# Performance work log

Measured on AMD Instinct MI355X. Metric: run time of the kernel, lower is better.

## Reference

```python
import jax, jax.numpy as jnp
import numpy as np
import math

B, L, D = 4, 2048, 512
H = 8
HD = D // H
K1 = 64  # local_window_size
K2 = 64  # global_window_size


def semi_local_mask(seq_len):
    # Faithful to create_semi_local_mask: anti-diagonal band + global prefix, ANDed with causal tril.
    i = jnp.arange(seq_len)[:, None]
    j = jnp.arange(seq_len)[None, :]
    band = (i + j >= seq_len - K1) & (i + j <= seq_len)
    glob = (j <= K2) & (j <= seq_len - i)
    causal = j <= i
    return (band | glob) & causal  # [L, L] bool


def setup_inputs() -> dict:
    key = jax.random.key(0)
    ks = jax.random.split(key, 8)
    def xavier(k, shape):
        fan_in, fan_out = shape[1], shape[0]
        lim = math.sqrt(6.0 / (fan_in + fan_out))
        return jax.random.uniform(k, shape, jnp.float32, -lim, lim)
    x = jax.random.normal(ks[0], (B, L, D), jnp.float32)
    w_qkv = xavier(ks[1], (3 * D, D)); b_qkv = jnp.zeros((3 * D,), jnp.float32)
    w_u = xavier(ks[2], (D, D));       b_u = jnp.zeros((D,), jnp.float32)
    w_out = xavier(ks[3], (D, D));     b_out = jnp.zeros((D,), jnp.float32)
    return {"x": x, "w_qkv": w_qkv, "b_qkv": b_qkv, "w_u": w_u, "b_u": b_u,
            "w_out": w_out, "b_out": b_out}


def reference(x, w_qkv, b_qkv, w_u, b_u, w_out, b_out):
    Bsz, Lq, Dm = x.shape
    qkv = (x @ w_qkv.T + b_qkv).reshape(Bsz, Lq, 3, H, HD)
    q, k, v = jnp.moveaxis(qkv, 2, 0)            # each [B, L, H, HD]
    q = jnp.transpose(q, (0, 2, 1, 3))           # [B, H, L, HD]
    k = jnp.transpose(k, (0, 2, 1, 3))
    v = jnp.transpose(v, (0, 2, 1, 3))
    u = x @ w_u.T + b_u                          # [B, L, D] (gate values)
    scale = 1.0 / math.sqrt(HD)
    scores = jnp.einsum('bhqd,bhkd->bhqk', q * scale, k)
    mask = semi_local_mask(Lq)                   # [L, L]
    scores = jnp.where(mask[None, None], scores, -jnp.inf)
    attn = jax.nn.softmax(scores, axis=-1)
    out = jnp.einsum('bhqk,bhkd->bhqd', attn, v)
    out = jnp.transpose(out, (0, 2, 1, 3)).reshape(Bsz, Lq, Dm)
    out = jax.nn.silu(out) * u
    return out @ w_out.T + b_out
```

## Files before the change

kernel.cpp:

```cpp
#include <hip/hip_runtime.h>
#include <hip/hip_bf16.h>

typedef __bf16 bf16x8 __attribute__((ext_vector_type(8)));
typedef float f32x4 __attribute__((ext_vector_type(4)));

#define B_ 4
#define L_ 2048
#define D_ 512
#define H_ 8
#define QS 2048
#define SP 72

#define SB0 __builtin_amdgcn_sched_barrier(0)
#define WAIT_VM(n) asm volatile("s_waitcnt vmcnt(" #n ")" ::: "memory")
#define WAIT_LGKM0 asm volatile("s_waitcnt lgkmcnt(0)" ::: "memory")

__device__ __forceinline__ void gl16(const __bf16* g, __bf16* l) {
  __builtin_amdgcn_global_load_lds(
      (const __attribute__((address_space(1))) void*)g,
      (__attribute__((address_space(3))) void*)l, 16, 0, 0);
}

__global__ __launch_bounds__(256) void cvt_pack(
    const float* __restrict__ x, const float* __restrict__ wq,
    const float* __restrict__ wu, const float* __restrict__ wo,
    const float* __restrict__ bq, const float* __restrict__ bu,
    __bf16* __restrict__ xb, __bf16* __restrict__ wcat,
    __bf16* __restrict__ wob, float* __restrict__ bcat)
{
  const int idx8 = blockIdx.x * 256 + threadIdx.x;
  const float* src; __bf16* dst; size_t so, dof;
  if (idx8 < 524288)      { src = x;  dst = xb;   so = (size_t)idx8 * 8;            dof = so; }
  else if (idx8 < 622592) { src = wq; dst = wcat; so = (size_t)(idx8 - 524288) * 8; dof = so; }
  else if (idx8 < 655360) { src = wu; dst = wcat; so = (size_t)(idx8 - 622592) * 8; dof = so + 786432; }
  else                    { src = wo; dst = wob;  so = (size_t)(idx8 - 655360) * 8; dof = so; }
  const float4 lo = *(const float4*)(src + so);
  const float4 hi = *(const float4*)(src + so + 4);
  bf16x8 r;
  r[0] = (__bf16)lo.x; r[1] = (__bf16)lo.y; r[2] = (__bf16)lo.z; r[3] = (__bf16)lo.w;
  r[4] = (__bf16)hi.x; r[5] = (__bf16)hi.y; r[6] = (__bf16)hi.z; r[7] = (__bf16)hi.w;
  *(bf16x8*)(dst + dof) = r;
  if (blockIdx.x == 0) {
#pragma unroll
    for (int e = 0; e < 8; ++e) {
      const int col = threadIdx.x * 8 + e;
      bcat[col] = (col < 1536) ? bq[col] : bu[col - 1536];
    }
  }
}

__global__ __launch_bounds__(256, 2) void gemm128(
    const __bf16* __restrict__ A, const __bf16* __restrict__ W,
    const float* __restrict__ bias, __bf16* __restrict__ C,
    int M, int N, int K)
{
  extern __shared__ char sm[];
  const int t = threadIdx.x;
  const int lane = t & 63;
  const int wave = t >> 6;
  const int wm = (wave >> 1) * 64;
  const int wn = (wave & 1) * 64;
  const int bm0 = blockIdx.x * 128;
  const int bn0 = blockIdx.y * 128;
  const int r = lane & 15, q = lane >> 4;
  const int nt = K >> 6;

  auto stage = [&](int kt, int p) {
#pragma unroll
    for (int j = 0; j < 4; ++j) {
      const int c = t + j * 256;
      const int row = c >> 3;
      const int cs = (c & 7) ^ (row & 7);
      gl16(A + (size_t)(bm0 + row) * K + kt * 64 + cs * 8,
           (__bf16*)(sm + p * 16384) + c * 8);
    }
#pragma unroll
    for (int j = 0; j < 4; ++j) {
      const int c = t + j * 256;
      const int row = c >> 3;
      const int cs = (c & 7) ^ (row & 7);
      gl16(W + (size_t)(bn0 + row) * K + kt * 64 + cs * 8,
           (__bf16*)(sm + 32768 + p * 16384) + c * 8);
    }
  };
  auto rdA = [&](int p, int mi, int ks) -> bf16x8 {
    const int row = wm + mi * 16 + r;
    const int byte = row * 128 + ((ks * 64 + q * 16) ^ ((row & 7) << 4));
    return *(const bf16x8*)(sm + p * 16384 + byte);
  };
  auto rdB = [&](int p, int ni, int ks) -> bf16x8 {
    const int row = wn + ni * 16 + r;
    const int byte = row * 128 + ((ks * 64 + q * 16) ^ ((row & 7) << 4));
    return *(const bf16x8*)(sm + 32768 + p * 16384 + byte);
  };

  f32x4 acc[4][4] = {};
  stage(0, 0);
  stage(1, 1);

  for (int kt = 0; kt < nt - 1; ++kt) {
    const int p = kt & 1;
    WAIT_VM(8);
    SB0; __builtin_amdgcn_s_barrier(); SB0;

    bf16x8 a[4][2], b01[2][2], b23[2][2];
#pragma unroll
    for (int mi = 0; mi < 4; ++mi) { a[mi][0] = rdA(p, mi, 0); a[mi][1] = rdA(p, mi, 1); }
#pragma unroll
    for (int ni = 0; ni < 2; ++ni) { b01[ni][0] = rdB(p, ni, 0); b01[ni][1] = rdB(p, ni, 1); }
    __builtin_amdgcn_s_setprio(1);
#pragma unroll
    for (int mi = 0; mi < 4; ++mi)
#pragma unroll
      for (int ni = 0; ni < 2; ++ni) {
        acc[mi][ni] = __builtin_amdgcn_mfma_f32_16x16x32_bf16(a[mi][0], b01[ni][0], acc[mi][ni], 0, 0, 0);
        acc[mi][ni] = __builtin_amdgcn_mfma_f32_16x16x32_bf16(a[mi][1], b01[ni][1], acc[mi][ni], 0, 0, 0);
      }
    __builtin_amdgcn_s_setprio(0);
#pragma unroll
    for (int ni = 0; ni < 2; ++ni) { b23[ni][0] = rdB(p, ni + 2, 0); b23[ni][1] = rdB(p, ni + 2, 1); }
    WAIT_LGKM0;
    SB0; __builtin_amdgcn_s_barrier(); SB0;
    if (kt + 2 < nt) stage(kt + 2, p);
    __builtin_amdgcn_s_setprio(1);
#pragma unroll
    for (int mi = 0; mi < 4; ++mi)
#pragma unroll
      for (int ni = 0; ni < 2; ++ni) {
        acc[mi][ni + 2] = __builtin_amdgcn_mfma_f32_16x16x32_bf16(a[mi][0], b23[ni][0], acc[mi][ni + 2], 0, 0, 0);
        acc[mi][ni + 2] = __builtin_amdgcn_mfma_f32_16x16x32_bf16(a[mi][1], b23[ni][1], acc[mi][ni + 2], 0, 0, 0);
      }
    __builtin_amdgcn_s_setprio(0);
  }

  {
    const int p = (nt - 1) & 1;
    const int cc = lane & 15, cq = lane >> 4;
    WAIT_VM(0);
    SB0; __builtin_amdgcn_s_barrier(); SB0;

    float bv[4];
#pragma unroll
    for (int ni = 0; ni < 4; ++ni) bv[ni] = bias[bn0 + wn + ni * 16 + cc];

    auto st = [&](int mi, int ni) {
      const int gcol = bn0 + wn + ni * 16 + cc;
#pragma unroll
      for (int rr = 0; rr < 4; ++rr) {
        const int grow = bm0 + wm + mi * 16 + cq * 4 + rr;
        C[(size_t)grow * N + gcol] = (__bf16)(acc[mi][ni][rr] + bv[ni]);
      }
    };

    bf16x8 a[4][2], b01[2][2], b23[2][2];
#pragma unroll
    for (int mi = 0; mi < 4; ++mi) { a[mi][0] = rdA(p, mi, 0); a[mi][1] = rdA(p, mi, 1); }
#pragma unroll
    for (int ni = 0; ni < 2; ++ni) { b01[ni][0] = rdB(p, ni, 0); b01[ni][1] = rdB(p, ni, 1); }
    __builtin_amdgcn_s_setprio(1);
#pragma unroll
    for (int mi = 0; mi < 4; ++mi)
#pragma unroll
      for (int ni = 0; ni < 2; ++ni) {
        acc[mi][ni] = __builtin_amdgcn_mfma_f32_16x16x32_bf16(a[mi][0], b01[ni][0], acc[mi][ni], 0, 0, 0);
        acc[mi][ni] = __builtin_amdgcn_mfma_f32_16x16x32_bf16(a[mi][1], b01[ni][1], acc[mi][ni], 0, 0, 0);
      }
    __builtin_amdgcn_s_setprio(0);
#pragma unroll
    for (int mi = 0; mi < 4; ++mi)
#pragma unroll
      for (int ni = 0; ni < 2; ++ni) st(mi, ni);

#pragma unroll
    for (int ni = 0; ni < 2; ++ni) { b23[ni][0] = rdB(p, ni + 2, 0); b23[ni][1] = rdB(p, ni + 2, 1); }
    __builtin_amdgcn_s_setprio(1);
#pragma unroll
    for (int mi = 0; mi < 4; ++mi)
#pragma unroll
      for (int ni = 0; ni < 2; ++ni) {
        acc[mi][ni + 2] = __builtin_amdgcn_mfma_f32_16x16x32_bf16(a[mi][0], b23[ni][0], acc[mi][ni + 2], 0, 0, 0);
        acc[mi][ni + 2] = __builtin_amdgcn_mfma_f32_16x16x32_bf16(a[mi][1], b23[ni][1], acc[mi][ni + 2], 0, 0, 0);
      }
    __builtin_amdgcn_s_setprio(0);
#pragma unroll
    for (int mi = 0; mi < 4; ++mi)
#pragma unroll
      for (int ni = 2; ni < 4; ++ni) st(mi, ni);
  }
}

__global__ __launch_bounds__(256, 2) void gemm_out(
    const __bf16* __restrict__ A, const __bf16* __restrict__ W,
    const float* __restrict__ bias, float* __restrict__ C)
{
  __shared__ char sm[49152];
  const int t = threadIdx.x;
  const int lane = t & 63;
  const int wave = t >> 6;
  const int wm = (wave >> 1) * 32;
  const int wn = (wave & 1) * 64;
  const int bm0 = blockIdx.x * 64;
  const int bn0 = blockIdx.y * 128;
  const int r = lane & 15, q = lane >> 4;
  const int K = 512, N = 512;

  auto stage = [&](int kt, int p) {
#pragma unroll
    for (int j = 0; j < 2; ++j) {
      const int c = t + j * 256;
      const int row = c >> 3;
      const int cs = (c & 7) ^ (row & 7);
      gl16(A + (size_t)(bm0 + row) * K + kt * 64 + cs * 8,
           (__bf16*)(sm + p * 8192) + c * 8);
    }
#pragma unroll
    for (int j = 0; j < 4; ++j) {
      const int c = t + j * 256;
      const int row = c >> 3;
      const int cs = (c & 7) ^ (row & 7);
      gl16(W + (size_t)(bn0 + row) * K + kt * 64 + cs * 8,
           (__bf16*)(sm + 16384 + p * 16384) + c * 8);
    }
  };
  auto rdA = [&](int p, int mi, int ks) -> bf16x8 {
    const int row = wm + mi * 16 + r;
    const int byte = row * 128 + ((ks * 64 + q * 16) ^ ((row & 7) << 4));
    return *(const bf16x8*)(sm + p * 8192 + byte);
  };
  auto rdB = [&](int p, int ni, int ks) -> bf16x8 {
    const int row = wn + ni * 16 + r;
    const int byte = row * 128 + ((ks * 64 + q * 16) ^ ((row & 7) << 4));
    return *(const bf16x8*)(sm + 16384 + p * 16384 + byte);
  };

  f32x4 acc[2][4] = {};
  stage(0, 0);
  stage(1, 1);

  for (int kt = 0; kt < 7; ++kt) {
    const int p = kt & 1;
    WAIT_VM(6);
    SB0; __builtin_amdgcn_s_barrier(); SB0;

    bf16x8 a[2][2], b01[2][2], b23[2][2];
#pragma unroll
    for (int mi = 0; mi < 2; ++mi) { a[mi][0] = rdA(p, mi, 0); a[mi][1] = rdA(p, mi, 1); }
#pragma unroll
    for (int ni = 0; ni < 2; ++ni) { b01[ni][0] = rdB(p, ni, 0); b01[ni][1] = rdB(p, ni, 1); }
    __builtin_amdgcn_s_setprio(1);
#pragma unroll
    for (int mi = 0; mi < 2; ++mi)
#pragma unroll
      for (int ni = 0; ni < 2; ++ni) {
        acc[mi][ni] = __builtin_amdgcn_mfma_f32_16x16x32_bf16(a[mi][0], b01[ni][0], acc[mi][ni], 0, 0, 0);
        acc[mi][ni] = __builtin_amdgcn_mfma_f32_16x16x32_bf16(a[mi][1], b01[ni][1], acc[mi][ni], 0, 0, 0);
      }
    __builtin_amdgcn_s_setprio(0);
#pragma unroll
    for (int ni = 0; ni < 2; ++ni) { b23[ni][0] = rdB(p, ni + 2, 0); b23[ni][1] = rdB(p, ni + 2, 1); }
    WAIT_LGKM0;
    SB0; __builtin_amdgcn_s_barrier(); SB0;
    if (kt + 2 < 8) stage(kt + 2, p);
    __builtin_amdgcn_s_setprio(1);
#pragma unroll
    for (int mi = 0; mi < 2; ++mi)
#pragma unroll
      for (int ni = 0; ni < 2; ++ni) {
        acc[mi][ni + 2] = __builtin_amdgcn_mfma_f32_16x16x32_bf16(a[mi][0], b23[ni][0], acc[mi][ni + 2], 0, 0, 0);
        acc[mi][ni + 2] = __builtin_amdgcn_mfma_f32_16x16x32_bf16(a[mi][1], b23[ni][1], acc[mi][ni + 2], 0, 0, 0);
      }
    __builtin_amdgcn_s_setprio(0);
  }

  {
    const int p = 1;
    const int cc = lane & 15, cq = lane >> 4;
    WAIT_VM(0);
    SB0; __builtin_amdgcn_s_barrier(); SB0;

    float bv[4];
#pragma unroll
    for (int ni = 0; ni < 4; ++ni) bv[ni] = bias[bn0 + wn + ni * 16 + cc];

    auto st = [&](int mi, int ni) {
      const int gcol = bn0 + wn + ni * 16 + cc;
#pragma unroll
      for (int rr = 0; rr < 4; ++rr) {
        const int grow = bm0 + wm + mi * 16 + cq * 4 + rr;
        C[(size_t)grow * N + gcol] = acc[mi][ni][rr] + bv[ni];
      }
    };

    bf16x8 a[2][2], b01[2][2], b23[2][2];
#pragma unroll
    for (int mi = 0; mi < 2; ++mi) { a[mi][0] = rdA(p, mi, 0); a[mi][1] = rdA(p, mi, 1); }
#pragma unroll
    for (int ni = 0; ni < 2; ++ni) { b01[ni][0] = rdB(p, ni, 0); b01[ni][1] = rdB(p, ni, 1); }
    __builtin_amdgcn_s_setprio(1);
#pragma unroll
    for (int mi = 0; mi < 2; ++mi)
#pragma unroll
      for (int ni = 0; ni < 2; ++ni) {
        acc[mi][ni] = __builtin_amdgcn_mfma_f32_16x16x32_bf16(a[mi][0], b01[ni][0], acc[mi][ni], 0, 0, 0);
        acc[mi][ni] = __builtin_amdgcn_mfma_f32_16x16x32_bf16(a[mi][1], b01[ni][1], acc[mi][ni], 0, 0, 0);
      }
    __builtin_amdgcn_s_setprio(0);
#pragma unroll
    for (int mi = 0; mi < 2; ++mi)
#pragma unroll
      for (int ni = 0; ni < 2; ++ni) st(mi, ni);

#pragma unroll
    for (int ni = 0; ni < 2; ++ni) { b23[ni][0] = rdB(p, ni + 2, 0); b23[ni][1] = rdB(p, ni + 2, 1); }
    __builtin_amdgcn_s_setprio(1);
#pragma unroll
    for (int mi = 0; mi < 2; ++mi)
#pragma unroll
      for (int ni = 0; ni < 2; ++ni) {
        acc[mi][ni + 2] = __builtin_amdgcn_mfma_f32_16x16x32_bf16(a[mi][0], b23[ni][0], acc[mi][ni + 2], 0, 0, 0);
        acc[mi][ni + 2] = __builtin_amdgcn_mfma_f32_16x16x32_bf16(a[mi][1], b23[ni][1], acc[mi][ni + 2], 0, 0, 0);
      }
    __builtin_amdgcn_s_setprio(0);
#pragma unroll
    for (int mi = 0; mi < 2; ++mi)
#pragma unroll
      for (int ni = 2; ni < 4; ++ni) st(mi, ni);
  }
}

__global__ __launch_bounds__(512) void attn_tile(
    const __bf16* __restrict__ qu,
    __bf16* __restrict__ g)
{
  const int qt = blockIdx.x, h = blockIdx.y, b = blockIdx.z;
  const int t = threadIdx.x;
  const int lane = t & 63;
  const int w = t >> 6;
  const int q0 = qt * 128, qmax = q0 + 127;
  const size_t bL = (size_t)b * L_;

  __shared__ __bf16 lK[4096];
  __shared__ __bf16 lV[64 * SP];
  __shared__ __bf16 Pb[128 * SP];

  const int cq = lane >> 4, cc = lane & 15;
  const int krow_st = t >> 3, kgb8 = t & 7;

  bf16x8 aq0, aq1;
  {
    const __bf16* qsrc = qu + (bL + q0 + w * 16 + cc) * QS + h * 64 + cq * 8;
    bf16x8 t0 = *(const bf16x8*)qsrc;
    bf16x8 t1 = *(const bf16x8*)(qsrc + 32);
#pragma unroll
    for (int e = 0; e < 8; ++e) {
      aq0[e] = (__bf16)((float)t0[e] * 0.125f);
      aq1[e] = (__bf16)((float)t1[e] * 0.125f);
    }
  }

  float mreg[4], lreg[4];
#pragma unroll
  for (int rr = 0; rr < 4; ++rr) { mreg[rr] = -1e30f; lreg[rr] = 0.f; }
  f32x4 acc_o[4] = {};

  int clist[8]; int ncl = 0;
  clist[ncl++] = 0;
  if (qmax >= 64) clist[ncl++] = 64;
  {
    int lo = 1984 - qmax; if (lo < 0) lo = 0; lo &= ~63;
    const int hik = min(qmax, 2048 - q0);
    for (int c = lo; c <= hik; c += 64)
      if (c >= 128) clist[ncl++] = c;
  }

  bf16x8 k0r, var;
  {
    const __bf16* src = qu + (bL + clist[0] + krow_st) * QS + 512 + h * 64;
    k0r = *(const bf16x8*)(src + kgb8 * 8);
    const __bf16* vsrc = qu + (bL + clist[0] + lane) * QS + 1024 + h * 64 + w * 8;
    var = *(const bf16x8*)vsrc;
  }

  for (int ci = 0; ci < ncl; ++ci) {
    const int c0 = clist[ci];
    const bool thin = (c0 == 64) && (qmax <= 1856);
    const bool fast0 = (c0 == 0) && (q0 >= 64) && (qmax + 63 <= 2048);

    WAIT_VM(0);
    SB0; __builtin_amdgcn_s_barrier(); SB0;
    {
      char* lkb = (char*)lK;
      const int sw = (krow_st & 7) << 4;
      *(bf16x8*)(lkb + ((krow_st * 128 + kgb8 * 16) ^ sw)) = k0r;
#pragma unroll
      for (int e = 0; e < 8; ++e)
        lV[(w * 8 + e) * SP + lane] = var[e];
    }
    if (ci + 1 < ncl) {
      const int cn = clist[ci + 1];
      const __bf16* src = qu + (bL + cn + krow_st) * QS + 512 + h * 64;
      k0r = *(const bf16x8*)(src + kgb8 * 8);
      const __bf16* vsrc = qu + (bL + cn + lane) * QS + 1024 + h * 64 + w * 8;
      var = *(const bf16x8*)vsrc;
    }
    WAIT_LGKM0;
    SB0; __builtin_amdgcn_s_barrier(); SB0;

    f32x4 s[4];
    {
      const char* lkb = (const char*)lK;
      auto qk = [&](int nt) {
        const int krow = nt * 16 + cc;
        const int sw = (krow & 7) << 4;
        bf16x8 bk0 = *(const bf16x8*)(lkb + ((krow * 128 + cq * 16) ^ sw));
        bf16x8 bk1 = *(const bf16x8*)(lkb + ((krow * 128 + 64 + cq * 16) ^ sw));
        f32x4 a = {};
        a = __builtin_amdgcn_mfma_f32_16x16x32_bf16(aq0, bk0, a, 0, 0, 0);
        a = __builtin_amdgcn_mfma_f32_16x16x32_bf16(aq1, bk1, a, 0, 0, 0);
        s[nt] = a;
      };
      qk(0);
      if (!thin) { qk(1); qk(2); qk(3); }
    }

    if (!fast0) {
      const int ntm = thin ? 1 : 4;
      if (c0 >= 128) {
        for (int nt = 0; nt < 4; ++nt) {
          if (nt >= ntm) break;
#pragma unroll
          for (int rr = 0; rr < 4; ++rr) {
            const int i = q0 + w * 16 + cq * 4 + rr;
            const int j = c0 + nt * 16 + cc;
            const int ij = i + j;
            const bool valid = (j <= i) && (ij >= 1984) && (ij <= 2048);
            s[nt][rr] = valid ? s[nt][rr] : -1e30f;
          }
        }
      } else {
        for (int nt = 0; nt < 4; ++nt) {
          if (nt >= ntm) break;
#pragma unroll
          for (int rr = 0; rr < 4; ++rr) {
            const int i = q0 + w * 16 + cq * 4 + rr;
            const int j = c0 + nt * 16 + cc;
            const int ij = i + j;
            const bool valid = (j <= i) &&
                ((ij >= 1984 && ij <= 2048) || (j <= 64 && ij <= 2048));
            s[nt][rr] = valid ? s[nt][rr] : -1e30f;
          }
        }
      }
    }

    f32x4 pm;
#pragma unroll
    for (int rr = 0; rr < 4; ++rr) pm[rr] = s[0][rr];
    if (!thin) {
#pragma unroll
      for (int rr = 0; rr < 4; ++rr)
        pm[rr] = fmaxf(fmaxf(pm[rr], s[1][rr]), fmaxf(s[2][rr], s[3][rr]));
    }
#pragma unroll
    for (int m = 1; m < 16; m <<= 1) {
#pragma unroll
      for (int rr = 0; rr < 4; ++rr)
        pm[rr] = fmaxf(pm[rr], __shfl_xor(pm[rr], m, 64));
    }
    float corr[4];
#pragma unroll
    for (int rr = 0; rr < 4; ++rr) {
      const float nm = fmaxf(mreg[rr], pm[rr]);
      corr[rr] = __expf(mreg[rr] - nm);
      mreg[rr] = nm;
    }

    f32x4 ps = {};
    if (thin) {
#pragma unroll
      for (int rr = 0; rr < 4; ++rr) {
        const float p = __expf(s[0][rr] - mreg[rr]);
        ps[rr] += p;
        const int prow = (w * 16 + cq * 4 + rr) * SP;
        Pb[prow + cc] = (__bf16)p;
        Pb[prow + 16 + cc] = (__bf16)0.f;
      }
    } else {
#pragma unroll
      for (int nt = 0; nt < 4; ++nt) {
#pragma unroll
        for (int rr = 0; rr < 4; ++rr) {
          const float p = __expf(s[nt][rr] - mreg[rr]);
          ps[rr] += p;
          Pb[(w * 16 + cq * 4 + rr) * SP + nt * 16 + cc] = (__bf16)p;
        }
      }
    }
#pragma unroll
    for (int m = 1; m < 16; m <<= 1) {
#pragma unroll
      for (int rr = 0; rr < 4; ++rr)
        ps[rr] += __shfl_xor(ps[rr], m, 64);
    }
#pragma unroll
    for (int rr = 0; rr < 4; ++rr) lreg[rr] = lreg[rr] * corr[rr] + ps[rr];

    {
      bf16x8 pa0 = *(const bf16x8*)(Pb + (w * 16 + cc) * SP + cq * 8);
      if (thin) {
#pragma unroll
        for (int dt = 0; dt < 4; ++dt) {
#pragma unroll
          for (int rr = 0; rr < 4; ++rr) acc_o[dt][rr] *= corr[rr];
          bf16x8 vb0 = *(const bf16x8*)(lV + (dt * 16 + cc) * SP + cq * 8);
          acc_o[dt] = __builtin_amdgcn_mfma_f32_16x16x32_bf16(pa0, vb0, acc_o[dt], 0, 0, 0);
        }
      } else {
        bf16x8 pa1 = *(const bf16x8*)(Pb + (w * 16 + cc) * SP + 32 + cq * 8);
#pragma unroll
        for (int dt = 0; dt < 4; ++dt) {
#pragma unroll
          for (int rr = 0; rr < 4; ++rr) acc_o[dt][rr] *= corr[rr];
          bf16x8 vb0 = *(const bf16x8*)(lV + (dt * 16 + cc) * SP + cq * 8);
          bf16x8 vb1 = *(const bf16x8*)(lV + (dt * 16 + cc) * SP + 32 + cq * 8);
          acc_o[dt] = __builtin_amdgcn_mfma_f32_16x16x32_bf16(pa0, vb0, acc_o[dt], 0, 0, 0);
          acc_o[dt] = __builtin_amdgcn_mfma_f32_16x16x32_bf16(pa1, vb1, acc_o[dt], 0, 0, 0);
        }
      }
    }
  }

#pragma unroll
  for (int dt = 0; dt < 4; ++dt) {
#pragma unroll
    for (int rr = 0; rr < 4; ++rr) {
      const int row16 = cq * 4 + rr;
      const size_t qrow = bL + q0 + w * 16 + row16;
      const int d = dt * 16 + cc;
      const float o = acc_o[dt][rr] / fmaxf(lreg[rr], 1e-30f);
      const float uv = (float)qu[qrow * QS + 1536 + h * 64 + d];
      g[qrow * D_ + h * 64 + d] = (__bf16)(o / (1.f + __expf(-o)) * uv);
    }
  }
}

extern "C" void kernel_launch(void* const* d_in, const int* in_sizes, int n_in,
                              void* d_out, int out_size, void* d_ws, size_t ws_size,
                              hipStream_t stream) {
  const float* x     = (const float*)d_in[0];
  const float* w_qkv = (const float*)d_in[1];
  const float* b_qkv = (const float*)d_in[2];
  const float* w_u   = (const float*)d_in[3];
  const float* b_u   = (const float*)d_in[4];
  const float* w_out = (const float*)d_in[5];
  const float* b_out = (const float*)d_in[6];
  float* out = (float*)d_out;

  char* ws = (char*)d_ws;
  __bf16* xb   = (__bf16*)ws;
  __bf16* wcat = (__bf16*)(ws + 8388608);
  __bf16* wob  = (__bf16*)(ws + 10485760);
  float*  bcat = (float*) (ws + 11010048);
  __bf16* qu   = (__bf16*)(ws + 11018240);
  __bf16* gb   = (__bf16*)(ws + 44572672);

  static bool attr_done = []() {
    hipFuncSetAttribute((const void*)gemm128,
                        hipFuncAttributeMaxDynamicSharedMemorySize, 65536);
    return true;
  }();
  (void)attr_done;

  cvt_pack<<<dim3(2688), dim3(256), 0, stream>>>(
      x, w_qkv, w_u, w_out, b_qkv, b_u, xb, wcat, wob, bcat);
  gemm128<<<dim3(64, 16), dim3(256), 65536, stream>>>(
      xb, wcat, bcat, qu, 8192, 2048, 512);
  attn_tile<<<dim3(L_ / 128, H_, B_), dim3(512), 0, stream>>>(qu, gb);
  gemm_out<<<dim3(128, 4), dim3(256), 0, stream>>>(
      gb, wob, b_out, out);
}
```

Before: 136.7 us.

## Fuse fp32-to-bf16 conversion of x into the QKV/U projection GEMM

Instead of a separate pass that converts x to bf16 in workspace, the projection GEMM now loads fp32 x rows into registers, converts them, and writes bf16 into LDS, with a register double-buffer and a fully unrolled K loop. The conversion kernel only handles the weights now. This removes an 8 MB bf16 write and reread of x. The cost is that each x tile is read as fp32 by all 16 column blocks (twice the bytes per load), plus extra register pressure and VALU work inside the GEMM.

```diff
diff --git a/kernel.cpp b/kernel.cpp
--- a/kernel.cpp
+++ b/kernel.cpp
@@ -22,18 +22,16 @@
 }
 
 __global__ __launch_bounds__(256) void cvt_pack(
-    const float* __restrict__ x, const float* __restrict__ wq,
-    const float* __restrict__ wu, const float* __restrict__ wo,
-    const float* __restrict__ bq, const float* __restrict__ bu,
-    __bf16* __restrict__ xb, __bf16* __restrict__ wcat,
+    const float* __restrict__ wq, const float* __restrict__ wu,
+    const float* __restrict__ wo, const float* __restrict__ bq,
+    const float* __restrict__ bu, __bf16* __restrict__ wcat,
     __bf16* __restrict__ wob, float* __restrict__ bcat)
 {
   const int idx8 = blockIdx.x * 256 + threadIdx.x;
   const float* src; __bf16* dst; size_t so, dof;
-  if (idx8 < 524288)      { src = x;  dst = xb;   so = (size_t)idx8 * 8;            dof = so; }
-  else if (idx8 < 622592) { src = wq; dst = wcat; so = (size_t)(idx8 - 524288) * 8; dof = so; }
-  else if (idx8 < 655360) { src = wu; dst = wcat; so = (size_t)(idx8 - 622592) * 8; dof = so + 786432; }
-  else                    { src = wo; dst = wob;  so = (size_t)(idx8 - 655360) * 8; dof = so; }
+  if (idx8 < 98304)       { src = wq; dst = wcat; so = (size_t)idx8 * 8;            dof = so; }
+  else if (idx8 < 131072) { src = wu; dst = wcat; so = (size_t)(idx8 - 98304) * 8;  dof = so + 786432; }
+  else                    { src = wo; dst = wob;  so = (size_t)(idx8 - 131072) * 8; dof = so; }
   const float4 lo = *(const float4*)(src + so);
   const float4 hi = *(const float4*)(src + so + 4);
   bf16x8 r;
@@ -49,10 +47,9 @@
   }
 }
 
-__global__ __launch_bounds__(256, 2) void gemm128(
-    const __bf16* __restrict__ A, const __bf16* __restrict__ W,
-    const float* __restrict__ bias, __bf16* __restrict__ C,
-    int M, int N, int K)
+__global__ __launch_bounds__(256, 2) void gemm_qkvu(
+    const float* __restrict__ X, const __bf16* __restrict__ W,
+    const float* __restrict__ bias, __bf16* __restrict__ C)
 {
   extern __shared__ char sm[];
   const int t = threadIdx.x;
@@ -63,24 +60,39 @@
   const int bm0 = blockIdx.x * 128;
   const int bn0 = blockIdx.y * 128;
   const int r = lane & 15, q = lane >> 4;
-  const int nt = K >> 6;
-
-  auto stage = [&](int kt, int p) {
+  const int N = 2048;
+
+  auto stageA = [&](int kt, f32x4 (&ar)[8]) {
 #pragma unroll
     for (int j = 0; j < 4; ++j) {
       const int c = t + j * 256;
       const int row = c >> 3;
       const int cs = (c & 7) ^ (row & 7);
-      gl16(A + (size_t)(bm0 + row) * K + kt * 64 + cs * 8,
-           (__bf16*)(sm + p * 16384) + c * 8);
-    }
+      const float* src = X + (size_t)(bm0 + row) * 512 + kt * 64 + cs * 8;
+      ar[2 * j]     = *(const f32x4*)src;
+      ar[2 * j + 1] = *(const f32x4*)(src + 4);
+    }
+  };
+  auto stageB = [&](int kt, int p) {
 #pragma unroll
     for (int j = 0; j < 4; ++j) {
       const int c = t + j * 256;
       const int row = c >> 3;
       const int cs = (c & 7) ^ (row & 7);
-      gl16(W + (size_t)(bn0 + row) * K + kt * 64 + cs * 8,
+      gl16(W + (size_t)(bn0 + row) * 512 + kt * 64 + cs * 8,
            (__bf16*)(sm + 32768 + p * 16384) + c * 8);
+    }
+  };
+  auto writeA = [&](int p, f32x4 (&ar)[8]) {
+#pragma unroll
+    for (int j = 0; j < 4; ++j) {
+      const int c = t + j * 256;
+      bf16x8 v;
+      v[0] = (__bf16)ar[2 * j][0];     v[1] = (__bf16)ar[2 * j][1];
+      v[2] = (__bf16)ar[2 * j][2];     v[3] = (__bf16)ar[2 * j][3];
+      v[4] = (__bf16)ar[2 * j + 1][0]; v[5] = (__bf16)ar[2 * j + 1][1];
+      v[6] = (__bf16)ar[2 * j + 1][2]; v[7] = (__bf16)ar[2 * j + 1][3];
+      *(bf16x8*)((__bf16*)(sm + p * 16384) + (size_t)c * 8) = v;
     }
   };
   auto rdA = [&](int p, int mi, int ks) -> bf16x8 {
@@ -95,12 +107,16 @@
   };
 
   f32x4 acc[4][4] = {};
-  stage(0, 0);
-  stage(1, 1);
-
-  for (int kt = 0; kt < nt - 1; ++kt) {
+  f32x4 ar0[8], ar1[8];
+
+  stageA(0, ar0); stageB(0, 0);
+  stageA(1, ar1); stageB(1, 1);
+
+  auto body = [&](int kt, f32x4 (&ar)[8]) {
     const int p = kt & 1;
-    WAIT_VM(8);
+    writeA(p, ar);
+    WAIT_VM(12);
+    WAIT_LGKM0;
     SB0; __builtin_amdgcn_s_barrier(); SB0;
 
     bf16x8 a[4][2], b01[2][2], b23[2][2];
@@ -121,7 +137,7 @@
     for (int ni = 0; ni < 2; ++ni) { b23[ni][0] = rdB(p, ni + 2, 0); b23[ni][1] = rdB(p, ni + 2, 1); }
     WAIT_LGKM0;
     SB0; __builtin_amdgcn_s_barrier(); SB0;
-    if (kt + 2 < nt) stage(kt + 2, p);
+    if (kt + 2 < 8) { stageA(kt + 2, ar); stageB(kt + 2, p); }
     __builtin_amdgcn_s_setprio(1);
 #pragma unroll
     for (int mi = 0; mi < 4; ++mi)
@@ -131,12 +147,19 @@
         acc[mi][ni + 2] = __builtin_amdgcn_mfma_f32_16x16x32_bf16(a[mi][1], b23[ni][1], acc[mi][ni + 2], 0, 0, 0);
       }
     __builtin_amdgcn_s_setprio(0);
-  }
+  };
+
+  body(0, ar0); body(1, ar1);
+  body(2, ar0); body(3, ar1);
+  body(4, ar0); body(5, ar1);
+  body(6, ar0);
 
   {
-    const int p = (nt - 1) & 1;
+    const int p = 1;
     const int cc = lane & 15, cq = lane >> 4;
+    writeA(p, ar1);
     WAIT_VM(0);
+    WAIT_LGKM0;
     SB0; __builtin_amdgcn_s_barrier(); SB0;
 
     float bv[4];
@@ -557,24 +580,23 @@
   float* out = (float*)d_out;
 
   char* ws = (char*)d_ws;
-  __bf16* xb   = (__bf16*)ws;
-  __bf16* wcat = (__bf16*)(ws + 8388608);
-  __bf16* wob  = (__bf16*)(ws + 10485760);
-  float*  bcat = (float*) (ws + 11010048);
-  __bf16* qu   = (__bf16*)(ws + 11018240);
-  __bf16* gb   = (__bf16*)(ws + 44572672);
+  __bf16* wcat = (__bf16*)ws;
+  __bf16* wob  = (__bf16*)(ws + 2097152);
+  float*  bcat = (float*) (ws + 2621440);
+  __bf16* qu   = (__bf16*)(ws + 2629632);
+  __bf16* gb   = (__bf16*)(ws + 36184064);
 
   static bool attr_done = []() {
-    hipFuncSetAttribute((const void*)gemm128,
+    hipFuncSetAttribute((const void*)gemm_qkvu,
                         hipFuncAttributeMaxDynamicSharedMemorySize, 65536);
     return true;
   }();
   (void)attr_done;
 
-  cvt_pack<<<dim3(2688), dim3(256), 0, stream>>>(
-      x, w_qkv, w_u, w_out, b_qkv, b_u, xb, wcat, wob, bcat);
-  gemm128<<<dim3(64, 16), dim3(256), 65536, stream>>>(
-      xb, wcat, bcat, qu, 8192, 2048, 512);
+  cvt_pack<<<dim3(640), dim3(256), 0, stream>>>(
+      w_qkv, w_u, w_out, b_qkv, b_u, wcat, wob, bcat);
+  gemm_qkvu<<<dim3(64, 16), dim3(256), 65536, stream>>>(
+      x, wcat, bcat, qu);
   attn_tile<<<dim3(L_ / 128, H_, B_), dim3(512), 0, stream>>>(qu, gb);
   gemm_out<<<dim3(128, 4), dim3(256), 0, stream>>>(
       gb, wob, b_out, out);
```

Measured after the change: 141.2 us. 1.03x slower.
